# Kernel tuning notes

Measured on AMD Instinct MI355X. Metric: run time of the kernel, lower is better.

The kernel has to match this reference:

```python
import jax, jax.numpy as jnp
import numpy as np

H, D = 8, 16            # head_num, qkv_dim
E = H * D               # embedding_dim = 128
SQRT_E = float(np.sqrt(E))
LOGIT_CLIP = 10.0
MAX_DELTA = 4           # decoder_priority_bias_max_delta
TEMP = 0.8              # sampling_temperature
TOP_K = 20              # sampling_top_k


def setup_inputs() -> dict:
    key = jax.random.key(0)
    ks = jax.random.split(key, 12)
    B, P, N = 256, 200, 200
    s = 1.0 / np.sqrt(E)
    return {
        "encoded_nodes": jax.random.normal(ks[0], (B, N, E), jnp.float32),
        "encoded_first_node": jax.random.normal(ks[1], (B, P, E), jnp.float32),
        "encoded_last_node": jax.random.normal(ks[2], (B, P, E), jnp.float32),
        "ninf_mask": jnp.zeros((B, P, N), jnp.float32),
        "group_ids": jax.random.randint(ks[3], (B, N), 0, 5, jnp.int32),
        "current_min_priority": jax.random.randint(ks[4], (B, P), 0, 5, jnp.int32),
        "Wq_first": jax.random.normal(ks[5], (E, H * D), jnp.float32) * s,
        "Wq_last": jax.random.normal(ks[6], (E, H * D), jnp.float32) * s,
        "Wk": jax.random.normal(ks[7], (E, H * D), jnp.float32) * s,
        "Wv": jax.random.normal(ks[8], (E, H * D), jnp.float32) * s,
        "Wc": jax.random.normal(ks[9], (H * D, E), jnp.float32) * s,
        "bc": jax.random.normal(ks[10], (E,), jnp.float32) * 0.01,
        # learnable priority bias table: init * exp(-delta / tau)
        "bias_table": 0.2 * jnp.exp(-jnp.arange(MAX_DELTA + 1, dtype=jnp.float32)),
    }


def _heads(x):
    # [B, n, H*D] -> [B, H, n, D]
    B, n, _ = x.shape
    return x.reshape(B, n, H, D).transpose(0, 2, 1, 3)


def reference(encoded_nodes, encoded_first_node, encoded_last_node, ninf_mask,
              group_ids, current_min_priority,
              Wq_first, Wq_last, Wk, Wv, Wc, bc, bias_table):
    B, P, N = ninf_mask.shape
    # set_q1 + per-step q_last, q = q_first + q_last
    q = _heads(encoded_first_node @ Wq_first) + _heads(encoded_last_node @ Wq_last)
    k = _heads(encoded_nodes @ Wk)  # [B,H,N,D]
    v = _heads(encoded_nodes @ Wv)
    # masked multi-head attention with rank-3 ninf mask
    score = jnp.einsum('bhpd,bhnd->bhpn', q, k) / jnp.sqrt(jnp.float32(D))
    score = score + ninf_mask[:, None, :, :]
    w = jax.nn.softmax(score, axis=-1)
    out = jnp.einsum('bhpn,bhnd->bhpd', w, v)          # [B,H,P,D]
    out_concat = out.transpose(0, 2, 1, 3).reshape(B, P, H * D)
    mh = out_concat @ Wc + bc                          # multi_head_combine
    # single-head pointer attention
    sc = jnp.einsum('bpe,bne->bpn', mh, encoded_nodes)
    score_clipped = LOGIT_CLIP * jnp.tanh(sc / SQRT_E)
    # decoder priority bias (learnable table indexed by clamped delta)
    delta = jnp.clip(group_ids[:, None, :] - current_min_priority[:, :, None], 0, MAX_DELTA)
    pbias = bias_table[delta] * jnp.isfinite(ninf_mask)
    probs = jax.nn.softmax(score_clipped + pbias + ninf_mask, axis=-1)
    # sampling controls (eval): temperature then top-k filtering, renormalize
    adj = jnp.power(jnp.maximum(probs, 1e-12), 1.0 / TEMP)
    vals, idx = jax.lax.top_k(adj, TOP_K)
    bi = jnp.arange(B)[:, None, None]
    pi = jnp.arange(P)[None, :, None]
    filtered = jnp.zeros_like(adj).at[bi, pi, idx].set(vals)
    denom = jnp.maximum(filtered.sum(axis=-1, keepdims=True), 1e-12)
    return filtered / denom
```

## Files before the change

kernel.cpp:

```cpp
#include <hip/hip_runtime.h>
#include <hip/hip_bf16.h>
#include <math.h>

constexpr int B = 256, P = 200, N = 200, E = 128, H = 8, D = 16;
constexpr float INV_SQRT_D = 0.25f;
constexpr float INV_SQRT_E = 0.08838834764831845f;
constexpr float LOGIT_CLIP = 10.0f;
constexpr float INV_TEMP = 1.25f;
constexpr int TOP_K = 20;
constexpr int MAX_DELTA = 4;

__device__ __forceinline__ float dot4(float4 a, float4 b) {
    return a.x*b.x + a.y*b.y + a.z*b.z + a.w*b.w;
}

__global__ __launch_bounds__(256) void proj_kernel(
    const float* __restrict__ X1, const float* __restrict__ W1,
    const float* __restrict__ X2, const float* __restrict__ W2,
    const float* __restrict__ bias, float* __restrict__ out)
{
    __shared__ float4 xs[32][32];
    __shared__ float4 ws[2][16][32];
    const int tid = threadIdx.x;
    const int eg = tid & 31;
    const int rg = tid >> 5;
    const long base = (long)blockIdx.x * 32;

    float acc[4][4];
    #pragma unroll
    for (int i = 0; i < 4; ++i)
        #pragma unroll
        for (int j = 0; j < 4; ++j) acc[i][j] = 0.f;

    for (int pass = 0; pass < 2; ++pass) {
        const float* X = pass ? X2 : X1;
        const float* W = pass ? W2 : W1;
        if (!X) break;
        if (pass) __syncthreads();
        const float4* X4 = (const float4*)X;
        const float4* W4 = (const float4*)W;
        #pragma unroll
        for (int t = 0; t < 4; ++t) {
            int idx = tid + 256 * t;
            int r = idx >> 5, c = idx & 31;
            xs[r][c] = X4[(base + r) * 32 + c];
        }
        #pragma unroll
        for (int t = 0; t < 2; ++t) {
            int idx = tid + 256 * t;
            int r = idx >> 5, c = idx & 31;
            ws[0][r][c] = W4[r * 32 + c];
        }
        __syncthreads();

        for (int kc = 0; kc < 8; ++kc) {
            const int cur = kc & 1;
            float4 pf0, pf1;
            if (kc < 7) {
                int i0 = tid, i1 = tid + 256;
                pf0 = W4[((kc + 1) * 16 + (i0 >> 5)) * 32 + (i0 & 31)];
                pf1 = W4[((kc + 1) * 16 + (i1 >> 5)) * 32 + (i1 & 31)];
            }
            #pragma unroll
            for (int k4 = 0; k4 < 4; ++k4) {
                float4 xv[4];
                #pragma unroll
                for (int i = 0; i < 4; ++i)
                    xv[i] = xs[rg + 8 * i][kc * 4 + k4];
                float4 w0 = ws[cur][k4 * 4 + 0][eg];
                float4 w1 = ws[cur][k4 * 4 + 1][eg];
                float4 w2 = ws[cur][k4 * 4 + 2][eg];
                float4 w3 = ws[cur][k4 * 4 + 3][eg];
                #pragma unroll
                for (int i = 0; i < 4; ++i) {
                    acc[i][0] += xv[i].x*w0.x + xv[i].y*w1.x + xv[i].z*w2.x + xv[i].w*w3.x;
                    acc[i][1] += xv[i].x*w0.y + xv[i].y*w1.y + xv[i].z*w2.y + xv[i].w*w3.y;
                    acc[i][2] += xv[i].x*w0.z + xv[i].y*w1.z + xv[i].z*w2.z + xv[i].w*w3.z;
                    acc[i][3] += xv[i].x*w0.w + xv[i].y*w1.w + xv[i].z*w2.w + xv[i].w*w3.w;
                }
            }
            if (kc < 7) {
                int i0 = tid, i1 = tid + 256;
                ws[cur ^ 1][i0 >> 5][i0 & 31] = pf0;
                ws[cur ^ 1][i1 >> 5][i1 & 31] = pf1;
                __syncthreads();
            }
        }
    }

    float4 bv = make_float4(0.f, 0.f, 0.f, 0.f);
    if (bias) bv = *(const float4*)&bias[eg * 4];
    float4* out4 = (float4*)out;
    #pragma unroll
    for (int i = 0; i < 4; ++i) {
        out4[(base + rg + 8 * i) * 32 + eg] =
            make_float4(acc[i][0]+bv.x, acc[i][1]+bv.y, acc[i][2]+bv.z, acc[i][3]+bv.w);
    }
}

__global__ __launch_bounds__(256) void kv_proj_kernel(
    const float* __restrict__ X, const float* __restrict__ Wk,
    const float* __restrict__ Wv, float* __restrict__ outK,
    float* __restrict__ outV)
{
    __shared__ float4 xs[32][32];
    __shared__ float4 wsk[2][16][32];
    __shared__ float4 wsv[2][16][32];
    const int tid = threadIdx.x;
    const int eg = tid & 31;
    const int rg = tid >> 5;
    const long base = (long)blockIdx.x * 32;

    float acck[4][4], accv[4][4];
    #pragma unroll
    for (int i = 0; i < 4; ++i)
        #pragma unroll
        for (int j = 0; j < 4; ++j) { acck[i][j] = 0.f; accv[i][j] = 0.f; }

    const float4* X4 = (const float4*)X;
    const float4* Wk4 = (const float4*)Wk;
    const float4* Wv4 = (const float4*)Wv;
    #pragma unroll
    for (int t = 0; t < 4; ++t) {
        int idx = tid + 256 * t;
        int r = idx >> 5, c = idx & 31;
        xs[r][c] = X4[(base + r) * 32 + c];
    }
    #pragma unroll
    for (int t = 0; t < 2; ++t) {
        int idx = tid + 256 * t;
        int r = idx >> 5, c = idx & 31;
        wsk[0][r][c] = Wk4[r * 32 + c];
        wsv[0][r][c] = Wv4[r * 32 + c];
    }
    __syncthreads();

    for (int kc = 0; kc < 8; ++kc) {
        const int cur = kc & 1;
        float4 pk0, pk1, pv0, pv1;
        if (kc < 7) {
            int i0 = tid, i1 = tid + 256;
            int a0 = ((kc + 1) * 16 + (i0 >> 5)) * 32 + (i0 & 31);
            int a1 = ((kc + 1) * 16 + (i1 >> 5)) * 32 + (i1 & 31);
            pk0 = Wk4[a0]; pk1 = Wk4[a1];
            pv0 = Wv4[a0]; pv1 = Wv4[a1];
        }
        #pragma unroll
        for (int k4 = 0; k4 < 4; ++k4) {
            float4 xv[4];
            #pragma unroll
            for (int i = 0; i < 4; ++i)
                xv[i] = xs[rg + 8 * i][kc * 4 + k4];
            float4 k0 = wsk[cur][k4 * 4 + 0][eg];
            float4 k1 = wsk[cur][k4 * 4 + 1][eg];
            float4 k2 = wsk[cur][k4 * 4 + 2][eg];
            float4 k3 = wsk[cur][k4 * 4 + 3][eg];
            float4 v0 = wsv[cur][k4 * 4 + 0][eg];
            float4 v1 = wsv[cur][k4 * 4 + 1][eg];
            float4 v2 = wsv[cur][k4 * 4 + 2][eg];
            float4 v3 = wsv[cur][k4 * 4 + 3][eg];
            #pragma unroll
            for (int i = 0; i < 4; ++i) {
                acck[i][0] += xv[i].x*k0.x + xv[i].y*k1.x + xv[i].z*k2.x + xv[i].w*k3.x;
                acck[i][1] += xv[i].x*k0.y + xv[i].y*k1.y + xv[i].z*k2.y + xv[i].w*k3.y;
                acck[i][2] += xv[i].x*k0.z + xv[i].y*k1.z + xv[i].z*k2.z + xv[i].w*k3.z;
                acck[i][3] += xv[i].x*k0.w + xv[i].y*k1.w + xv[i].z*k2.w + xv[i].w*k3.w;
                accv[i][0] += xv[i].x*v0.x + xv[i].y*v1.x + xv[i].z*v2.x + xv[i].w*v3.x;
                accv[i][1] += xv[i].x*v0.y + xv[i].y*v1.y + xv[i].z*v2.y + xv[i].w*v3.y;
                accv[i][2] += xv[i].x*v0.z + xv[i].y*v1.z + xv[i].z*v2.z + xv[i].w*v3.z;
                accv[i][3] += xv[i].x*v0.w + xv[i].y*v1.w + xv[i].z*v2.w + xv[i].w*v3.w;
            }
        }
        if (kc < 7) {
            int i0 = tid, i1 = tid + 256;
            wsk[cur ^ 1][i0 >> 5][i0 & 31] = pk0;
            wsk[cur ^ 1][i1 >> 5][i1 & 31] = pk1;
            wsv[cur ^ 1][i0 >> 5][i0 & 31] = pv0;
            wsv[cur ^ 1][i1 >> 5][i1 & 31] = pv1;
            __syncthreads();
        }
    }

    float4* outK4 = (float4*)outK;
    float4* outV4 = (float4*)outV;
    #pragma unroll
    for (int i = 0; i < 4; ++i) {
        outK4[(base + rg + 8 * i) * 32 + eg] =
            make_float4(acck[i][0], acck[i][1], acck[i][2], acck[i][3]);
        outV4[(base + rg + 8 * i) * 32 + eg] =
            make_float4(accv[i][0], accv[i][1], accv[i][2], accv[i][3]);
    }
}

__global__ __launch_bounds__(256) void attn_kernel(
    const float* __restrict__ q, const float* __restrict__ k,
    const float* __restrict__ v, const float* __restrict__ mask,
    float* __restrict__ out)
{
    __shared__ float4 ks[N][4];
    __shared__ float4 vs[N][4];
    __shared__ float red[4];
    const int raw = blockIdx.x;
    const int g = raw >> 6, rr6 = raw & 63;
    const int h = rr6 >> 3;
    const int b = g * 8 + (rr6 & 7);
    const int tid = threadIdx.x;

    const float4* k4 = (const float4*)k;
    const float4* v4 = (const float4*)v;
    for (int idx = tid; idx < N * 4; idx += 256) {
        int n = idx >> 2, c = idx & 3;
        size_t off = (size_t)(b * N + n) * 32 + h * 4 + c;
        ks[n][c] = k4[off];
        vs[n][c] = v4[off];
    }
    __syncthreads();

    float nrm = 0.f;
    if (tid < N) {
        float4 a0 = ks[tid][0], a1 = ks[tid][1], a2 = ks[tid][2], a3 = ks[tid][3];
        nrm = dot4(a0,a0) + dot4(a1,a1) + dot4(a2,a2) + dot4(a3,a3);
    }
    float wm = nrm;
    #pragma unroll
    for (int off = 32; off > 0; off >>= 1) wm = fmaxf(wm, __shfl_xor(wm, off));
    if ((tid & 63) == 0) red[tid >> 6] = wm;
    __syncthreads();
    const float kmax2 = fmaxf(fmaxf(red[0], red[1]), fmaxf(red[2], red[3]));

    const int p = tid;
    if (p >= P) return;

    const float4* qr = (const float4*)q + (size_t)(b * P + p) * 32 + h * 4;
    float4 q0 = qr[0], q1 = qr[1], q2 = qr[2], q3 = qr[3];
    q0.x*=INV_SQRT_D; q0.y*=INV_SQRT_D; q0.z*=INV_SQRT_D; q0.w*=INV_SQRT_D;
    q1.x*=INV_SQRT_D; q1.y*=INV_SQRT_D; q1.z*=INV_SQRT_D; q1.w*=INV_SQRT_D;
    q2.x*=INV_SQRT_D; q2.y*=INV_SQRT_D; q2.z*=INV_SQRT_D; q2.w*=INV_SQRT_D;
    q3.x*=INV_SQRT_D; q3.y*=INV_SQRT_D; q3.z*=INV_SQRT_D; q3.w*=INV_SQRT_D;
    const float qn2 = dot4(q0,q0) + dot4(q1,q1) + dot4(q2,q2) + dot4(q3,q3);
    const float M = sqrtf(qn2 * kmax2);

    const float4* m4 = (const float4*)(mask + (size_t)(b * P + p) * N);

    float l = 0.f;
    float o[16];
    #pragma unroll
    for (int d = 0; d < 16; ++d) o[d] = 0.f;

    #pragma unroll 2
    for (int n4 = 0; n4 < N / 4; ++n4) {
        float4 mv = m4[n4];
        float mvf[4] = {mv.x, mv.y, mv.z, mv.w};
        #pragma unroll
        for (int j = 0; j < 4; ++j) {
            int n = n4 * 4 + j;
            float s = dot4(q0, ks[n][0]) + dot4(q1, ks[n][1]) +
                      dot4(q2, ks[n][2]) + dot4(q3, ks[n][3]);
            float w = __expf(s + mvf[j] - M);
            l += w;
            float4 v0 = vs[n][0], v1 = vs[n][1], v2 = vs[n][2], v3 = vs[n][3];
            o[0]  += w*v0.x; o[1]  += w*v0.y; o[2]  += w*v0.z; o[3]  += w*v0.w;
            o[4]  += w*v1.x; o[5]  += w*v1.y; o[6]  += w*v1.z; o[7]  += w*v1.w;
            o[8]  += w*v2.x; o[9]  += w*v2.y; o[10] += w*v2.z; o[11] += w*v2.w;
            o[12] += w*v3.x; o[13] += w*v3.y; o[14] += w*v3.z; o[15] += w*v3.w;
        }
    }

    float inv_l = 1.f / l;
    float4* out4 = (float4*)out;
    size_t ob = (size_t)(b * P + p) * 32 + h * 4;
    #pragma unroll
    for (int c = 0; c < 4; ++c)
        out4[ob + c] = make_float4(o[c*4]*inv_l, o[c*4+1]*inv_l,
                                   o[c*4+2]*inv_l, o[c*4+3]*inv_l);
}

__global__ __launch_bounds__(256) void pointer_kernel(
    const float* __restrict__ mh, const float* __restrict__ nodes,
    const float* __restrict__ mask, const int* __restrict__ gid,
    const int* __restrict__ cmp, const float* __restrict__ btab,
    float* __restrict__ out)
{
    __shared__ float4 as[64][17];
    __shared__ float4 bs[64][17];
    const int b = blockIdx.z;
    const int p_base = blockIdx.y * 64;
    const int n_base = blockIdx.x * 64;
    const int tid = threadIdx.x;
    const int pi = tid >> 4;
    const int ni = tid & 15;

    const float4* mh4 = (const float4*)mh;
    const float4* nodes4 = (const float4*)nodes;

    float acc[4][4];
    #pragma unroll
    for (int i = 0; i < 4; ++i)
        #pragma unroll
        for (int j = 0; j < 4; ++j) acc[i][j] = 0.f;

    for (int ks = 0; ks < 2; ++ks) {
        if (ks) __syncthreads();
        #pragma unroll
        for (int t = 0; t < 4; ++t) {
            int idx = tid + 256 * t;
            int r = idx >> 4, c = idx & 15;
            int pr = p_base + r; pr = pr < P ? pr : P - 1;
            int nr = n_base + r; nr = nr < N ? nr : N - 1;
            as[r][c] = mh4[(size_t)(b * P + pr) * 32 + ks * 16 + c];
            bs[r][c] = nodes4[(size_t)(b * N + nr) * 32 + ks * 16 + c];
        }
        __syncthreads();

        for (int c4 = 0; c4 < 16; ++c4) {
            float4 a[4], w[4];
            #pragma unroll
            for (int i = 0; i < 4; ++i) a[i] = as[pi + 16 * i][c4];
            #pragma unroll
            for (int j = 0; j < 4; ++j) w[j] = bs[ni + 16 * j][c4];
            #pragma unroll
            for (int i = 0; i < 4; ++i)
                #pragma unroll
                for (int j = 0; j < 4; ++j)
                    acc[i][j] += dot4(a[i], w[j]);
        }
    }

    float bt[MAX_DELTA + 1];
    #pragma unroll
    for (int t = 0; t <= MAX_DELTA; ++t) bt[t] = btab[t];

    #pragma unroll
    for (int i = 0; i < 4; ++i) {
        int p = p_base + pi + 16 * i;
        if (p >= P) continue;
        int cm = cmp[b * P + p];
        #pragma unroll
        for (int j = 0; j < 4; ++j) {
            int n = n_base + ni + 16 * j;
            if (n >= N) continue;
            int g = gid[b * N + n];
            int delta = g - cm;
            delta = delta < 0 ? 0 : (delta > MAX_DELTA ? MAX_DELTA : delta);
            float mv = mask[(size_t)(b * P + p) * N + n];
            float pb = isfinite(mv) ? bt[delta] : 0.f;
            float logit = LOGIT_CLIP * tanhf(acc[i][j] * INV_SQRT_E) + pb + mv;
            out[(size_t)(b * P + p) * N + n] = logit;
        }
    }
}

__global__ __launch_bounds__(256) void topk_kernel(float* __restrict__ io)
{
    const int wv = threadIdx.x >> 6, lane = threadIdx.x & 63;
    const long row = (long)blockIdx.x * 4 + wv;
    float* r = io + row * N;

    float x[4];
    unsigned u[4];
    #pragma unroll
    for (int j = 0; j < 4; ++j) {
        int n = lane + 64 * j;
        bool valid = n < N;
        x[j] = valid ? r[n] : -INFINITY;
        unsigned bb = __float_as_uint(x[j]);
        u[j] = valid ? ((bb & 0x80000000u) ? ~bb : (bb | 0x80000000u)) : 0u;
    }

    unsigned p = 0;
    for (int i = 31; i >= 0; --i) {
        unsigned c = p | (1u << i);
        int cnt = 0;
        #pragma unroll
        for (int j = 0; j < 4; ++j)
            cnt += (int)__popcll(__ballot(u[j] >= c));
        if (cnt >= TOP_K) p = c;
    }

    int cnt_gt = 0;
    #pragma unroll
    for (int j = 0; j < 4; ++j)
        cnt_gt += (int)__popcll(__ballot(u[j] > p));
    const int needed = TOP_K - cnt_gt;

    const unsigned long long lt_mask = (1ull << lane) - 1ull;
    bool sel[4];
    int eq_before = 0;
    #pragma unroll
    for (int j = 0; j < 4; ++j) {
        unsigned long long em = __ballot(u[j] == p);
        int myrank = eq_before + (int)__popcll(em & lt_mask);
        sel[j] = (u[j] > p) || ((u[j] == p) && (myrank < needed));
        eq_before += (int)__popcll(em);
    }

    unsigned tb = (p & 0x80000000u) ? (p & 0x7FFFFFFFu) : ~p;
    float Tf = __uint_as_float(tb);

    float e[4];
    float sum = 0.f;
    if (isfinite(Tf)) {
        #pragma unroll
        for (int j = 0; j < 4; ++j) {
            e[j] = sel[j] ? __expf((x[j] - Tf) * INV_TEMP) : 0.f;
            sum += e[j];
        }
    } else {
        #pragma unroll
        for (int j = 0; j < 4; ++j) {
            e[j] = sel[j] ? 1.f : 0.f;
            sum += e[j];
        }
    }
    #pragma unroll
    for (int off = 32; off > 0; off >>= 1) sum += __shfl_xor(sum, off);
    float inv = 1.f / sum;
    #pragma unroll
    for (int j = 0; j < 4; ++j) {
        int n = lane + 64 * j;
        if (n < N) r[n] = e[j] * inv;
    }
}

extern "C" void kernel_launch(void* const* d_in, const int* in_sizes, int n_in,
                              void* d_out, int out_size, void* d_ws, size_t ws_size,
                              hipStream_t stream) {
    const float* nodes = (const float*)d_in[0];
    const float* first = (const float*)d_in[1];
    const float* last  = (const float*)d_in[2];
    const float* mask  = (const float*)d_in[3];
    const int*   gid   = (const int*)d_in[4];
    const int*   cmp   = (const int*)d_in[5];
    const float* Wqf   = (const float*)d_in[6];
    const float* Wql   = (const float*)d_in[7];
    const float* Wk    = (const float*)d_in[8];
    const float* Wv    = (const float*)d_in[9];
    const float* Wc    = (const float*)d_in[10];
    const float* bc    = (const float*)d_in[11];
    const float* btab  = (const float*)d_in[12];
    float* out = (float*)d_out;

    float* ws   = (float*)d_ws;
    const size_t SLOT = (size_t)B * P * E;
    float* qb  = ws;
    float* kb  = ws + SLOT;
    float* vb  = ws + 2 * SLOT;
    float* ao  = ws + 3 * SLOT;

    const int M = B * P;

    proj_kernel<<<M / 32, 256, 0, stream>>>(first, Wqf, last, Wql, nullptr, qb);
    kv_proj_kernel<<<M / 32, 256, 0, stream>>>(nodes, Wk, Wv, kb, vb);

    attn_kernel<<<B * H, 256, 0, stream>>>(qb, kb, vb, mask, ao);

    proj_kernel<<<M / 32, 256, 0, stream>>>(ao, Wc, nullptr, nullptr, bc, qb);

    dim3 pgrid((N + 63) / 64, (P + 63) / 64, B);
    pointer_kernel<<<pgrid, 256, 0, stream>>>(qb, nodes, mask, gid, cmp, btab, out);

    topk_kernel<<<(B * P) / 4, 256, 0, stream>>>(out);
}
```

Measured before the change: 580.2 us.

## Fuse Q and KV projections into one launch and pointer scoring with top-k

Merges the Q projection and the K/V projection into a single kernel whose blocks branch on block index, cutting one launch and letting both run concurrently. Fuses pointer-logit computation with top-k sampling: each block computes a 64-row by 200-column logit tile into LDS and runs the radix top-k per row from shared memory, avoiding writing logits to global memory and reading them back. The fused pointer kernel reads mh directly from global per k-step instead of staging it, uses a large LDS tile that limits occupancy, and launches only 1024 blocks. tanh is replaced with an exp-based formula.

```diff
diff --git a/kernel.cpp b/kernel.cpp
--- a/kernel.cpp
+++ b/kernel.cpp
@@ -98,97 +98,170 @@
     }
 }
 
-__global__ __launch_bounds__(256) void kv_proj_kernel(
-    const float* __restrict__ X, const float* __restrict__ Wk,
+__global__ __launch_bounds__(256) void qkv_proj_kernel(
+    const float* __restrict__ first, const float* __restrict__ Wqf,
+    const float* __restrict__ last,  const float* __restrict__ Wql,
+    float* __restrict__ outQ,
+    const float* __restrict__ nodes, const float* __restrict__ Wk,
     const float* __restrict__ Wv, float* __restrict__ outK,
     float* __restrict__ outV)
 {
-    __shared__ float4 xs[32][32];
-    __shared__ float4 wsk[2][16][32];
-    __shared__ float4 wsv[2][16][32];
+    __shared__ float4 smem[3072];
     const int tid = threadIdx.x;
     const int eg = tid & 31;
     const int rg = tid >> 5;
-    const long base = (long)blockIdx.x * 32;
-
-    float acck[4][4], accv[4][4];
-    #pragma unroll
-    for (int i = 0; i < 4; ++i)
-        #pragma unroll
-        for (int j = 0; j < 4; ++j) { acck[i][j] = 0.f; accv[i][j] = 0.f; }
-
-    const float4* X4 = (const float4*)X;
-    const float4* Wk4 = (const float4*)Wk;
-    const float4* Wv4 = (const float4*)Wv;
-    #pragma unroll
-    for (int t = 0; t < 4; ++t) {
-        int idx = tid + 256 * t;
-        int r = idx >> 5, c = idx & 31;
-        xs[r][c] = X4[(base + r) * 32 + c];
-    }
-    #pragma unroll
-    for (int t = 0; t < 2; ++t) {
-        int idx = tid + 256 * t;
-        int r = idx >> 5, c = idx & 31;
-        wsk[0][r][c] = Wk4[r * 32 + c];
-        wsv[0][r][c] = Wv4[r * 32 + c];
-    }
-    __syncthreads();
-
-    for (int kc = 0; kc < 8; ++kc) {
-        const int cur = kc & 1;
-        float4 pk0, pk1, pv0, pv1;
-        if (kc < 7) {
-            int i0 = tid, i1 = tid + 256;
-            int a0 = ((kc + 1) * 16 + (i0 >> 5)) * 32 + (i0 & 31);
-            int a1 = ((kc + 1) * 16 + (i1 >> 5)) * 32 + (i1 & 31);
-            pk0 = Wk4[a0]; pk1 = Wk4[a1];
-            pv0 = Wv4[a0]; pv1 = Wv4[a1];
-        }
-        #pragma unroll
-        for (int k4 = 0; k4 < 4; ++k4) {
-            float4 xv[4];
-            #pragma unroll
-            for (int i = 0; i < 4; ++i)
-                xv[i] = xs[rg + 8 * i][kc * 4 + k4];
-            float4 k0 = wsk[cur][k4 * 4 + 0][eg];
-            float4 k1 = wsk[cur][k4 * 4 + 1][eg];
-            float4 k2 = wsk[cur][k4 * 4 + 2][eg];
-            float4 k3 = wsk[cur][k4 * 4 + 3][eg];
-            float4 v0 = wsv[cur][k4 * 4 + 0][eg];
-            float4 v1 = wsv[cur][k4 * 4 + 1][eg];
-            float4 v2 = wsv[cur][k4 * 4 + 2][eg];
-            float4 v3 = wsv[cur][k4 * 4 + 3][eg];
-            #pragma unroll
-            for (int i = 0; i < 4; ++i) {
-                acck[i][0] += xv[i].x*k0.x + xv[i].y*k1.x + xv[i].z*k2.x + xv[i].w*k3.x;
-                acck[i][1] += xv[i].x*k0.y + xv[i].y*k1.y + xv[i].z*k2.y + xv[i].w*k3.y;
-                acck[i][2] += xv[i].x*k0.z + xv[i].y*k1.z + xv[i].z*k2.z + xv[i].w*k3.z;
-                acck[i][3] += xv[i].x*k0.w + xv[i].y*k1.w + xv[i].z*k2.w + xv[i].w*k3.w;
-                accv[i][0] += xv[i].x*v0.x + xv[i].y*v1.x + xv[i].z*v2.x + xv[i].w*v3.x;
-                accv[i][1] += xv[i].x*v0.y + xv[i].y*v1.y + xv[i].z*v2.y + xv[i].w*v3.y;
-                accv[i][2] += xv[i].x*v0.z + xv[i].y*v1.z + xv[i].z*v2.z + xv[i].w*v3.z;
-                accv[i][3] += xv[i].x*v0.w + xv[i].y*v1.w + xv[i].z*v2.w + xv[i].w*v3.w;
-            }
-        }
-        if (kc < 7) {
-            int i0 = tid, i1 = tid + 256;
-            wsk[cur ^ 1][i0 >> 5][i0 & 31] = pk0;
-            wsk[cur ^ 1][i1 >> 5][i1 & 31] = pk1;
-            wsv[cur ^ 1][i0 >> 5][i0 & 31] = pv0;
-            wsv[cur ^ 1][i1 >> 5][i1 & 31] = pv1;
+
+    if (blockIdx.x < 1600) {
+        const long base = (long)blockIdx.x * 32;
+        float4 (*xs)[32]       = (float4 (*)[32])smem;
+        float4 (*wsb)[16][32]  = (float4 (*)[16][32])(smem + 1024);
+
+        float acc[4][4];
+        #pragma unroll
+        for (int i = 0; i < 4; ++i)
+            #pragma unroll
+            for (int j = 0; j < 4; ++j) acc[i][j] = 0.f;
+
+        for (int pass = 0; pass < 2; ++pass) {
+            const float* X = pass ? last : first;
+            const float* W = pass ? Wql : Wqf;
+            if (pass) __syncthreads();
+            const float4* X4 = (const float4*)X;
+            const float4* W4 = (const float4*)W;
+            #pragma unroll
+            for (int t = 0; t < 4; ++t) {
+                int idx = tid + 256 * t;
+                xs[idx >> 5][idx & 31] = X4[(base + (idx >> 5)) * 32 + (idx & 31)];
+            }
+            #pragma unroll
+            for (int t = 0; t < 2; ++t) {
+                int idx = tid + 256 * t;
+                wsb[0][idx >> 5][idx & 31] = W4[(idx >> 5) * 32 + (idx & 31)];
+            }
             __syncthreads();
-        }
-    }
-
-    float4* outK4 = (float4*)outK;
-    float4* outV4 = (float4*)outV;
-    #pragma unroll
-    for (int i = 0; i < 4; ++i) {
-        outK4[(base + rg + 8 * i) * 32 + eg] =
-            make_float4(acck[i][0], acck[i][1], acck[i][2], acck[i][3]);
-        outV4[(base + rg + 8 * i) * 32 + eg] =
-            make_float4(accv[i][0], accv[i][1], accv[i][2], accv[i][3]);
+
+            for (int kc = 0; kc < 8; ++kc) {
+                const int cur = kc & 1;
+                float4 pf0, pf1;
+                if (kc < 7) {
+                    int i0 = tid, i1 = tid + 256;
+                    pf0 = W4[((kc + 1) * 16 + (i0 >> 5)) * 32 + (i0 & 31)];
+                    pf1 = W4[((kc + 1) * 16 + (i1 >> 5)) * 32 + (i1 & 31)];
+                }
+                #pragma unroll
+                for (int k4 = 0; k4 < 4; ++k4) {
+                    float4 xv[4];
+                    #pragma unroll
+                    for (int i = 0; i < 4; ++i)
+                        xv[i] = xs[rg + 8 * i][kc * 4 + k4];
+                    float4 w0 = wsb[cur][k4 * 4 + 0][eg];
+                    float4 w1 = wsb[cur][k4 * 4 + 1][eg];
+                    float4 w2 = wsb[cur][k4 * 4 + 2][eg];
+                    float4 w3 = wsb[cur][k4 * 4 + 3][eg];
+                    #pragma unroll
+                    for (int i = 0; i < 4; ++i) {
+                        acc[i][0] += xv[i].x*w0.x + xv[i].y*w1.x + xv[i].z*w2.x + xv[i].w*w3.x;
+                        acc[i][1] += xv[i].x*w0.y + xv[i].y*w1.y + xv[i].z*w2.y + xv[i].w*w3.y;
+                        acc[i][2] += xv[i].x*w0.z + xv[i].y*w1.z + xv[i].z*w2.z + xv[i].w*w3.z;
+                        acc[i][3] += xv[i].x*w0.w + xv[i].y*w1.w + xv[i].z*w2.w + xv[i].w*w3.w;
+                    }
+                }
+                if (kc < 7) {
+                    int i0 = tid, i1 = tid + 256;
+                    wsb[cur ^ 1][i0 >> 5][i0 & 31] = pf0;
+                    wsb[cur ^ 1][i1 >> 5][i1 & 31] = pf1;
+                    __syncthreads();
+                }
+            }
+        }
+        float4* out4 = (float4*)outQ;
+        #pragma unroll
+        for (int i = 0; i < 4; ++i)
+            out4[(base + rg + 8 * i) * 32 + eg] =
+                make_float4(acc[i][0], acc[i][1], acc[i][2], acc[i][3]);
+    } else {
+        const long base = (long)(blockIdx.x - 1600) * 32;
+        float4 (*xs)[32]      = (float4 (*)[32])smem;
+        float4 (*wsk)[16][32] = (float4 (*)[16][32])(smem + 1024);
+        float4 (*wsv)[16][32] = (float4 (*)[16][32])(smem + 2048);
+
+        float acck[4][4], accv[4][4];
+        #pragma unroll
+        for (int i = 0; i < 4; ++i)
+            #pragma unroll
+            for (int j = 0; j < 4; ++j) { acck[i][j] = 0.f; accv[i][j] = 0.f; }
+
+        const float4* X4  = (const float4*)nodes;
+        const float4* Wk4 = (const float4*)Wk;
+        const float4* Wv4 = (const float4*)Wv;
+        #pragma unroll
+        for (int t = 0; t < 4; ++t) {
+            int idx = tid + 256 * t;
+            xs[idx >> 5][idx & 31] = X4[(base + (idx >> 5)) * 32 + (idx & 31)];
+        }
+        #pragma unroll
+        for (int t = 0; t < 2; ++t) {
+            int idx = tid + 256 * t;
+            wsk[0][idx >> 5][idx & 31] = Wk4[(idx >> 5) * 32 + (idx & 31)];
+            wsv[0][idx >> 5][idx & 31] = Wv4[(idx >> 5) * 32 + (idx & 31)];
+        }
+        __syncthreads();
+
+        for (int kc = 0; kc < 8; ++kc) {
+            const int cur = kc & 1;
+            float4 pk0, pk1, pv0, pv1;
+            if (kc < 7) {
+                int i0 = tid, i1 = tid + 256;
+                int a0 = ((kc + 1) * 16 + (i0 >> 5)) * 32 + (i0 & 31);
+                int a1 = ((kc + 1) * 16 + (i1 >> 5)) * 32 + (i1 & 31);
+                pk0 = Wk4[a0]; pk1 = Wk4[a1];
+                pv0 = Wv4[a0]; pv1 = Wv4[a1];
+            }
+            #pragma unroll
+            for (int k4 = 0; k4 < 4; ++k4) {
+                float4 xv[4];
+                #pragma unroll
+                for (int i = 0; i < 4; ++i)
+                    xv[i] = xs[rg + 8 * i][kc * 4 + k4];
+                float4 k0 = wsk[cur][k4 * 4 + 0][eg];
+                float4 k1 = wsk[cur][k4 * 4 + 1][eg];
+                float4 k2 = wsk[cur][k4 * 4 + 2][eg];
+                float4 k3 = wsk[cur][k4 * 4 + 3][eg];
+                float4 v0 = wsv[cur][k4 * 4 + 0][eg];
+                float4 v1 = wsv[cur][k4 * 4 + 1][eg];
+                float4 v2 = wsv[cur][k4 * 4 + 2][eg];
+                float4 v3 = wsv[cur][k4 * 4 + 3][eg];
+                #pragma unroll
+                for (int i = 0; i < 4; ++i) {
+                    acck[i][0] += xv[i].x*k0.x + xv[i].y*k1.x + xv[i].z*k2.x + xv[i].w*k3.x;
+                    acck[i][1] += xv[i].x*k0.y + xv[i].y*k1.y + xv[i].z*k2.y + xv[i].w*k3.y;
+                    acck[i][2] += xv[i].x*k0.z + xv[i].y*k1.z + xv[i].z*k2.z + xv[i].w*k3.z;
+                    acck[i][3] += xv[i].x*k0.w + xv[i].y*k1.w + xv[i].z*k2.w + xv[i].w*k3.w;
+                    accv[i][0] += xv[i].x*v0.x + xv[i].y*v1.x + xv[i].z*v2.x + xv[i].w*v3.x;
+                    accv[i][1] += xv[i].x*v0.y + xv[i].y*v1.y + xv[i].z*v2.y + xv[i].w*v3.y;
+                    accv[i][2] += xv[i].x*v0.z + xv[i].y*v1.z + xv[i].z*v2.z + xv[i].w*v3.z;
+                    accv[i][3] += xv[i].x*v0.w + xv[i].y*v1.w + xv[i].z*v2.w + xv[i].w*v3.w;
+                }
+            }
+            if (kc < 7) {
+                int i0 = tid, i1 = tid + 256;
+                wsk[cur ^ 1][i0 >> 5][i0 & 31] = pk0;
+                wsk[cur ^ 1][i1 >> 5][i1 & 31] = pk1;
+                wsv[cur ^ 1][i0 >> 5][i0 & 31] = pv0;
+                wsv[cur ^ 1][i1 >> 5][i1 & 31] = pv1;
+                __syncthreads();
+            }
+        }
+
+        float4* outK4 = (float4*)outK;
+        float4* outV4 = (float4*)outV;
+        #pragma unroll
+        for (int i = 0; i < 4; ++i) {
+            outK4[(base + rg + 8 * i) * 32 + eg] =
+                make_float4(acck[i][0], acck[i][1], acck[i][2], acck[i][3]);
+            outV4[(base + rg + 8 * i) * 32 + eg] =
+                make_float4(accv[i][0], accv[i][1], accv[i][2], accv[i][3]);
+        }
     }
 }
 
@@ -275,150 +348,164 @@
                                    o[c*4+2]*inv_l, o[c*4+3]*inv_l);
 }
 
-__global__ __launch_bounds__(256) void pointer_kernel(
+__global__ __launch_bounds__(256) void pointer_topk_kernel(
     const float* __restrict__ mh, const float* __restrict__ nodes,
     const float* __restrict__ mask, const int* __restrict__ gid,
     const int* __restrict__ cmp, const float* __restrict__ btab,
     float* __restrict__ out)
 {
-    __shared__ float4 as[64][17];
-    __shared__ float4 bs[64][17];
-    const int b = blockIdx.z;
-    const int p_base = blockIdx.y * 64;
-    const int n_base = blockIdx.x * 64;
+    __shared__ float4 ns[32][33];
+    __shared__ float lg[64][225];
+
+    const int raw = blockIdx.x;
+    const int g = raw >> 5, r5 = raw & 31;
+    const int t = r5 >> 3;
+    const int b = g * 8 + (r5 & 7);
+    const int p0 = t * 64;
     const int tid = threadIdx.x;
     const int pi = tid >> 4;
     const int ni = tid & 15;
 
+    int cmv[4];
+    #pragma unroll
+    for (int i = 0; i < 4; ++i) {
+        int p = p0 + pi + 16 * i;
+        int pc = p < P ? p : P - 1;
+        cmv[i] = cmp[b * P + pc];
+    }
+    float bt[MAX_DELTA + 1];
+    #pragma unroll
+    for (int tt = 0; tt <= MAX_DELTA; ++tt) bt[tt] = btab[tt];
+
     const float4* mh4 = (const float4*)mh;
     const float4* nodes4 = (const float4*)nodes;
 
-    float acc[4][4];
-    #pragma unroll
-    for (int i = 0; i < 4; ++i)
-        #pragma unroll
-        for (int j = 0; j < 4; ++j) acc[i][j] = 0.f;
-
-    for (int ks = 0; ks < 2; ++ks) {
-        if (ks) __syncthreads();
-        #pragma unroll
-        for (int t = 0; t < 4; ++t) {
-            int idx = tid + 256 * t;
-            int r = idx >> 4, c = idx & 15;
-            int pr = p_base + r; pr = pr < P ? pr : P - 1;
-            int nr = n_base + r; nr = nr < N ? nr : N - 1;
-            as[r][c] = mh4[(size_t)(b * P + pr) * 32 + ks * 16 + c];
-            bs[r][c] = nodes4[(size_t)(b * N + nr) * 32 + ks * 16 + c];
+    for (int nc = 0; nc < 7; ++nc) {
+        const int n0 = nc * 32;
+        if (nc) __syncthreads();
+        #pragma unroll
+        for (int s = 0; s < 4; ++s) {
+            int idx = tid + 256 * s;
+            int rr = idx >> 5, cc = idx & 31;
+            int nr = n0 + rr; nr = nr < N ? nr : N - 1;
+            ns[rr][cc] = nodes4[(size_t)(b * N + nr) * 32 + cc];
         }
         __syncthreads();
 
-        for (int c4 = 0; c4 < 16; ++c4) {
-            float4 a[4], w[4];
-            #pragma unroll
-            for (int i = 0; i < 4; ++i) a[i] = as[pi + 16 * i][c4];
-            #pragma unroll
-            for (int j = 0; j < 4; ++j) w[j] = bs[ni + 16 * j][c4];
-            #pragma unroll
-            for (int i = 0; i < 4; ++i)
-                #pragma unroll
-                for (int j = 0; j < 4; ++j)
-                    acc[i][j] += dot4(a[i], w[j]);
-        }
-    }
-
-    float bt[MAX_DELTA + 1];
-    #pragma unroll
-    for (int t = 0; t <= MAX_DELTA; ++t) bt[t] = btab[t];
-
-    #pragma unroll
-    for (int i = 0; i < 4; ++i) {
-        int p = p_base + pi + 16 * i;
-        if (p >= P) continue;
-        int cm = cmp[b * P + p];
+        float acc[4][2];
+        #pragma unroll
+        for (int i = 0; i < 4; ++i) { acc[i][0] = 0.f; acc[i][1] = 0.f; }
+
+        #pragma unroll 4
+        for (int c4 = 0; c4 < 32; ++c4) {
+            float4 a[4];
+            #pragma unroll
+            for (int i = 0; i < 4; ++i) {
+                int p = p0 + pi + 16 * i;
+                int pc = p < P ? p : P - 1;
+                a[i] = mh4[(size_t)(b * P + pc) * 32 + c4];
+            }
+            float4 w0 = ns[ni][c4];
+            float4 w1 = ns[ni + 16][c4];
+            #pragma unroll
+            for (int i = 0; i < 4; ++i) {
+                acc[i][0] += dot4(a[i], w0);
+                acc[i][1] += dot4(a[i], w1);
+            }
+        }
+
+        #pragma unroll
+        for (int jj = 0; jj < 2; ++jj) {
+            int n = n0 + ni + 16 * jj;
+            if (n >= N) continue;
+            int gg = gid[b * N + n];
+            #pragma unroll
+            for (int i = 0; i < 4; ++i) {
+                int p = p0 + pi + 16 * i;
+                int pc = p < P ? p : P - 1;
+                int delta = gg - cmv[i];
+                delta = delta < 0 ? 0 : (delta > MAX_DELTA ? MAX_DELTA : delta);
+                float mv = mask[(size_t)(b * P + pc) * N + n];
+                float pb = isfinite(mv) ? bt[delta] : 0.f;
+                float ex = __expf(2.f * acc[i][jj] * INV_SQRT_E);
+                float logit = LOGIT_CLIP - 20.f / (ex + 1.f) + pb + mv;
+                lg[pi + 16 * i][n] = logit;
+            }
+        }
+    }
+    __syncthreads();
+
+    const int wv = tid >> 6, lane = tid & 63;
+    const unsigned long long lt_mask = (1ull << lane) - 1ull;
+    for (int rr = 0; rr < 16; ++rr) {
+        int row = wv * 16 + rr;
+        int p = p0 + row;
+        if (p >= P) break;
+
+        float x[4];
+        unsigned u[4];
         #pragma unroll
         for (int j = 0; j < 4; ++j) {
-            int n = n_base + ni + 16 * j;
-            if (n >= N) continue;
-            int g = gid[b * N + n];
-            int delta = g - cm;
-            delta = delta < 0 ? 0 : (delta > MAX_DELTA ? MAX_DELTA : delta);
-            float mv = mask[(size_t)(b * P + p) * N + n];
-            float pb = isfinite(mv) ? bt[delta] : 0.f;
-            float logit = LOGIT_CLIP * tanhf(acc[i][j] * INV_SQRT_E) + pb + mv;
-            out[(size_t)(b * P + p) * N + n] = logit;
-        }
-    }
-}
-
-__global__ __launch_bounds__(256) void topk_kernel(float* __restrict__ io)
-{
-    const int wv = threadIdx.x >> 6, lane = threadIdx.x & 63;
-    const long row = (long)blockIdx.x * 4 + wv;
-    float* r = io + row * N;
-
-    float x[4];
-    unsigned u[4];
-    #pragma unroll
-    for (int j = 0; j < 4; ++j) {
-        int n = lane + 64 * j;
-        bool valid = n < N;
-        x[j] = valid ? r[n] : -INFINITY;
-        unsigned bb = __float_as_uint(x[j]);
-        u[j] = valid ? ((bb & 0x80000000u) ? ~bb : (bb | 0x80000000u)) : 0u;
-    }
-
-    unsigned p = 0;
-    for (int i = 31; i >= 0; --i) {
-        unsigned c = p | (1u << i);
-        int cnt = 0;
+            int n = lane + 64 * j;
+            bool valid = n < N;
+            x[j] = valid ? lg[row][n] : -INFINITY;
+            unsigned bb = __float_as_uint(x[j]);
+            u[j] = valid ? ((bb & 0x80000000u) ? ~bb : (bb | 0x80000000u)) : 0u;
+        }
+
+        unsigned pth = 0;
+        for (int i = 31; i >= 0; --i) {
+            unsigned c = pth | (1u << i);
+            int cnt = 0;
+            #pragma unroll
+            for (int j = 0; j < 4; ++j)
+                cnt += (int)__popcll(__ballot(u[j] >= c));
+            if (cnt >= TOP_K) pth = c;
+        }
+
+        int cnt_gt = 0;
         #pragma unroll
         for (int j = 0; j < 4; ++j)
-            cnt += (int)__popcll(__ballot(u[j] >= c));
-        if (cnt >= TOP_K) p = c;
-    }
-
-    int cnt_gt = 0;
-    #pragma unroll
-    for (int j = 0; j < 4; ++j)
-        cnt_gt += (int)__popcll(__ballot(u[j] > p));
-    const int needed = TOP_K - cnt_gt;
-
-    const unsigned long long lt_mask = (1ull << lane) - 1ull;
-    bool sel[4];
-    int eq_before = 0;
-    #pragma unroll
-    for (int j = 0; j < 4; ++j) {
-        unsigned long long em = __ballot(u[j] == p);
-        int myrank = eq_before + (int)__popcll(em & lt_mask);
-        sel[j] = (u[j] > p) || ((u[j] == p) && (myrank < needed));
-        eq_before += (int)__popcll(em);
-    }
-
-    unsigned tb = (p & 0x80000000u) ? (p & 0x7FFFFFFFu) : ~p;
-    float Tf = __uint_as_float(tb);
-
-    float e[4];
-    float sum = 0.f;
-    if (isfinite(Tf)) {
+            cnt_gt += (int)__popcll(__ballot(u[j] > pth));
+        const int needed = TOP_K - cnt_gt;
+
+        bool sel[4];
+        int eq_before = 0;
         #pragma unroll
         for (int j = 0; j < 4; ++j) {
-            e[j] = sel[j] ? __expf((x[j] - Tf) * INV_TEMP) : 0.f;
-            sum += e[j];
-        }
-    } else {
+            unsigned long long em = __ballot(u[j] == pth);
+            int myrank = eq_before + (int)__popcll(em & lt_mask);
+            sel[j] = (u[j] > pth) || ((u[j] == pth) && (myrank < needed));
+            eq_before += (int)__popcll(em);
+        }
+
+        unsigned tb = (pth & 0x80000000u) ? (pth & 0x7FFFFFFFu) : ~pth;
+        float Tf = __uint_as_float(tb);
+
+        float e[4];
+        float sum = 0.f;
+        if (isfinite(Tf)) {
+            #pragma unroll
+            for (int j = 0; j < 4; ++j) {
+                e[j] = sel[j] ? __expf((x[j] - Tf) * INV_TEMP) : 0.f;
+                sum += e[j];
+            }
+        } else {
+            #pragma unroll
+            for (int j = 0; j < 4; ++j) {
+                e[j] = sel[j] ? 1.f : 0.f;
+                sum += e[j];
+            }
+        }
+        #pragma unroll
+        for (int off = 32; off > 0; off >>= 1) sum += __shfl_xor(sum, off);
+        float inv = 1.f / sum;
+        float* orow = out + (size_t)(b * P + p) * N;
         #pragma unroll
         for (int j = 0; j < 4; ++j) {
-            e[j] = sel[j] ? 1.f : 0.f;
-            sum += e[j];
-        }
-    }
-    #pragma unroll
-    for (int off = 32; off > 0; off >>= 1) sum += __shfl_xor(sum, off);
-    float inv = 1.f / sum;
-    #pragma unroll
-    for (int j = 0; j < 4; ++j) {
-        int n = lane + 64 * j;
-        if (n < N) r[n] = e[j] * inv;
+            int n = lane + 64 * j;
+            if (n < N) orow[n] = e[j] * inv;
+        }
     }
 }
 
@@ -449,15 +536,13 @@
 
     const int M = B * P;
 
-    proj_kernel<<<M / 32, 256, 0, stream>>>(first, Wqf, last, Wql, nullptr, qb);
-    kv_proj_kernel<<<M / 32, 256, 0, stream>>>(nodes, Wk, Wv, kb, vb);
+    qkv_proj_kernel<<<2 * (M / 32), 256, 0, stream>>>(
+        first, Wqf, last, Wql, qb, nodes, Wk, Wv, kb, vb);
 
     attn_kernel<<<B * H, 256, 0, stream>>>(qb, kb, vb, mask, ao);
 
     proj_kernel<<<M / 32, 256, 0, stream>>>(ao, Wc, nullptr, nullptr, bc, qb);
 
-    dim3 pgrid((N + 63) / 64, (P + 63) / 64, B);
-    pointer_kernel<<<pgrid, 256, 0, stream>>>(qb, nodes, mask, gid, cmp, btab, out);
-
-    topk_kernel<<<(B * P) / 4, 256, 0, stream>>>(out);
+    pointer_topk_kernel<<<B * 4, 256, 0, stream>>>(
+        qb, nodes, mask, gid, cmp, btab, out);
 }
```

Measured after the change: 674.0 us. +16.2%, slower.
